# Kernel optimization log

Hardware: AMD Instinct MI355X
Metric: run time of the kernel (lower is better)

The kernel has to match this reference:

```python
import jax, jax.numpy as jnp
import numpy as np

NUM_EDGES = 2_000_000
D = 32
NODE_NUM = 100_000


def setup_inputs() -> dict:
    key = jax.random.key(0)
    k1, k2 = jax.random.split(key)
    H = jax.random.normal(k1, (NUM_EDGES, D), dtype=jnp.float32)
    X_node = jax.random.randint(k2, (NUM_EDGES,), 0, NODE_NUM, dtype=jnp.int64)
    return {"H": H, "X_node": X_node, "node_num": NODE_NUM}


def reference(H, X_node, node_num):
    # Original builds a dense one-hot mask [node_num, num_edges] and does mm(mask, H).
    # That is exactly a scatter-sum of edge features H into node buckets by X_node.
    # (Note: torch.range(0, node_num-1) == arange(node_num) for integer node_num.)
    return jax.ops.segment_sum(H, X_node, num_segments=node_num)
```

## Files before the change

### kernel.cpp

```cpp
#include <hip/hip_runtime.h>
#include <hip/hip_bf16.h>


__global__ void AggrSum_46299747451335_kernel(const float* __restrict__ H,
                                              const int* __restrict__ X_node,
                                              float* __restrict__ out,
                                              int num_edges) {
    long long t = (long long)blockIdx.x * blockDim.x + threadIdx.x;
    long long total = (long long)num_edges * 32;
    if (t >= total) return;
    int edge = (int)(t >> 5);
    int col  = (int)(t & 31);
    int node = X_node[edge];
    float v = H[t];
    unsafeAtomicAdd(&out[(long long)node * 32 + col], v);
}

extern "C" void kernel_launch(void* const* d_in, const int* in_sizes, int n_in,
                              void* d_out, int out_size, void* d_ws, size_t ws_size,
                              hipStream_t stream) {
    const float* H      = (const float*)d_in[0];
    const int*   X_node = (const int*)d_in[1];
    float*       out    = (float*)d_out;

    const int num_edges = in_sizes[0] / 32;

    hipMemsetAsync(d_out, 0, (size_t)out_size * sizeof(float), stream);

    long long total_threads = (long long)num_edges * 32;
    int block = 256;
    long long grid = (total_threads + block - 1) / block;
    AggrSum_46299747451335_kernel<<<(dim3)(unsigned)grid, block, 0, stream>>>(
        H, X_node, out, num_edges);
}
```

Before: 458.6 us.

## Bucket edges by node bin and accumulate per-bin in shared memory

Replaces the global-atomic scatter-sum with a counting-sort pipeline: histogram edges into bins of 64 nodes, scan the counts, scatter edge indices into bin order, then have one block per bin sum H rows into shared-memory accumulators and write each output once. This removes the global float atomics and the output memset. In exchange it adds four launches, needs workspace, uses global atomics on the bin cursors (which is contended), and reads H at random row addresses. It falls back to the old kernel when the workspace or the size limits are not met.

```diff
diff --git a/kernel.cpp b/kernel.cpp
--- a/kernel.cpp
+++ b/kernel.cpp
@@ -1,6 +1,90 @@
 #include <hip/hip_runtime.h>
-#include <hip/hip_bf16.h>
 
+
+#define NPB   64
+#define SHIFT 6
+#define MAXBINS 2048
+
+__global__ void hist_kernel(const int* __restrict__ X, int E,
+                            int* __restrict__ counts, int nbins) {
+    extern __shared__ int h[];
+    for (int i = threadIdx.x; i < nbins; i += blockDim.x) h[i] = 0;
+    __syncthreads();
+    int stride = gridDim.x * blockDim.x;
+    for (long long i = (long long)blockIdx.x * blockDim.x + threadIdx.x; i < E;
+         i += stride)
+        atomicAdd(&h[X[i] >> SHIFT], 1);
+    __syncthreads();
+    for (int i = threadIdx.x; i < nbins; i += blockDim.x) {
+        int c = h[i];
+        if (c) atomicAdd(&counts[i], c);
+    }
+}
+
+__global__ void scan_kernel(const int* __restrict__ counts,
+                            int* __restrict__ start,
+                            int* __restrict__ cursor, int nbins) {
+    __shared__ int s[1024];
+    int tid = threadIdx.x;
+    int i0 = 2 * tid, i1 = 2 * tid + 1;
+    int c0 = (i0 < nbins) ? counts[i0] : 0;
+    int c1 = (i1 < nbins) ? counts[i1] : 0;
+    int pair = c0 + c1;
+    s[tid] = pair;
+    __syncthreads();
+    for (int off = 1; off < 1024; off <<= 1) {
+        int add = (tid >= off) ? s[tid - off] : 0;
+        __syncthreads();
+        s[tid] += add;
+        __syncthreads();
+    }
+    int excl = s[tid] - pair;
+    if (i0 < nbins) { start[i0] = excl;      cursor[i0] = excl;      }
+    if (i1 < nbins) { start[i1] = excl + c0; cursor[i1] = excl + c0; }
+}
+
+__global__ void scatter_kernel(const int* __restrict__ X, int E,
+                               int* __restrict__ cursor,
+                               unsigned* __restrict__ sorted) {
+    long long i = (long long)blockIdx.x * blockDim.x + threadIdx.x;
+    if (i >= E) return;
+    int node = X[(int)i];
+    int bin  = node >> SHIFT;
+    int pos  = atomicAdd(&cursor[bin], 1);
+    sorted[pos] = (unsigned)i | ((unsigned)(node & (NPB - 1)) << 24);
+}
+
+__global__ __launch_bounds__(256) void gather_kernel(
+        const float* __restrict__ H,
+        const unsigned* __restrict__ sorted,
+        const int* __restrict__ start,
+        float* __restrict__ out,
+        int E, int nbins, int nnodes) {
+    __shared__ float acc[NPB * 32];
+    int bin = blockIdx.x;
+    int s   = start[bin];
+    int end = (bin + 1 < nbins) ? start[bin + 1] : E;
+
+    for (int i = threadIdx.x; i < NPB * 32; i += 256) acc[i] = 0.0f;
+    __syncthreads();
+
+    int col  = threadIdx.x & 31;
+    int slot = threadIdx.x >> 5;
+    for (int i = s + slot; i < end; i += 8) {
+        unsigned p = sorted[i];
+        int edge  = (int)(p & 0xFFFFFFu);
+        int local = (int)(p >> 24);
+        float v = H[(long long)edge * 32 + col];
+        unsafeAtomicAdd(&acc[local * 32 + col], v);
+    }
+    __syncthreads();
+
+    int node_base = bin << SHIFT;
+    for (int i = threadIdx.x; i < NPB * 32; i += 256) {
+        int node = node_base + (i >> 5);
+        if (node < nnodes) out[(long long)node * 32 + (i & 31)] = acc[i];
+    }
+}
 
 __global__ void AggrSum_46299747451335_kernel(const float* __restrict__ H,
                                               const int* __restrict__ X_node,
@@ -24,12 +108,37 @@
     float*       out    = (float*)d_out;
 
     const int num_edges = in_sizes[0] / 32;
+    const int num_nodes = out_size / 32;
+    const int nbins     = (num_nodes + NPB - 1) >> SHIFT;
 
-    hipMemsetAsync(d_out, 0, (size_t)out_size * sizeof(float), stream);
+    size_t need = (size_t)3 * MAXBINS * sizeof(int)
+                + (size_t)num_edges * sizeof(unsigned);
 
-    long long total_threads = (long long)num_edges * 32;
-    int block = 256;
-    long long grid = (total_threads + block - 1) / block;
-    AggrSum_46299747451335_kernel<<<(dim3)(unsigned)grid, block, 0, stream>>>(
-        H, X_node, out, num_edges);
+    if (nbins <= MAXBINS && num_edges < (1 << 24) && ws_size >= need) {
+        char* ws = (char*)d_ws;
+        int*      counts = (int*)(ws);
+        int*      start  = (int*)(ws + (size_t)MAXBINS * sizeof(int));
+        int*      cursor = (int*)(ws + (size_t)2 * MAXBINS * sizeof(int));
+        unsigned* sorted = (unsigned*)(ws + (size_t)3 * MAXBINS * sizeof(int));
+
+        hipMemsetAsync(counts, 0, (size_t)nbins * sizeof(int), stream);
+
+        hist_kernel<<<256, 256, nbins * sizeof(int), stream>>>(
+            X_node, num_edges, counts, nbins);
+
+        scan_kernel<<<1, 1024, 0, stream>>>(counts, start, cursor, nbins);
+
+        int sgrid = (num_edges + 255) / 256;
+        scatter_kernel<<<sgrid, 256, 0, stream>>>(X_node, num_edges, cursor, sorted);
+
+        gather_kernel<<<nbins, 256, 0, stream>>>(
+            H, sorted, start, out, num_edges, nbins, num_nodes);
+    } else {
+        hipMemsetAsync(d_out, 0, (size_t)out_size * sizeof(float), stream);
+        long long total_threads = (long long)num_edges * 32;
+        int block = 256;
+        long long grid = (total_threads + block - 1) / block;
+        AggrSum_46299747451335_kernel<<<(dim3)(unsigned)grid, block, 0, stream>>>(
+            H, X_node, out, num_edges);
+    }
 }
```

Result: slower. 977.2 us (+113.1%).

## Replace global atomic scatter with binned counting sort and LDS gather-accumulate

Applied to the files above, without the earlier changes.

Edges are bucketed by node block (64 nodes per bin) through a histogram, a two-level scan and a scatter into a sorted index array. Each gather block then accumulates its bin's edges into shared memory and writes the output once, so the global float atomics and the output memset go away. The cost is several extra launches, workspace use, and random row gathers from H during the gather. If the workspace is too small or the sizes exceed the bounds, it falls back to the old atomic kernel.

```diff
diff --git a/kernel.cpp b/kernel.cpp
--- a/kernel.cpp
+++ b/kernel.cpp
@@ -1,6 +1,130 @@
 #include <hip/hip_runtime.h>
-#include <hip/hip_bf16.h>
 
+
+#define NPB     64
+#define SHIFT   6
+#define MAXBINS 2048
+#define NB      256
+
+__global__ __launch_bounds__(1024) void hist_kernel(
+        const int* __restrict__ X, int E, int chunk,
+        int* __restrict__ hist, int nbins) {
+    __shared__ int h[MAXBINS];
+    int blk = blockIdx.x;
+    for (int b = threadIdx.x; b < nbins; b += 1024) h[b] = 0;
+    __syncthreads();
+    int beg = blk * chunk;
+    int end = min(beg + chunk, E);
+    for (int i = beg + threadIdx.x; i < end; i += 1024)
+        atomicAdd(&h[X[i] >> SHIFT], 1);
+    __syncthreads();
+    for (int b = threadIdx.x; b < nbins; b += 1024)
+        hist[b * NB + blk] = h[b];
+}
+
+__global__ __launch_bounds__(256) void scanA_kernel(
+        int* __restrict__ hist, int* __restrict__ binTotal) {
+    __shared__ int s[NB];
+    int b = blockIdx.x, tid = threadIdx.x;
+    int v = hist[b * NB + tid];
+    s[tid] = v;
+    __syncthreads();
+    for (int off = 1; off < NB; off <<= 1) {
+        int add = (tid >= off) ? s[tid - off] : 0;
+        __syncthreads();
+        s[tid] += add;
+        __syncthreads();
+    }
+    hist[b * NB + tid] = s[tid] - v;
+    if (tid == NB - 1) binTotal[b] = s[NB - 1];
+}
+
+__global__ __launch_bounds__(1024) void scanB_kernel(
+        const int* __restrict__ binTotal, int* __restrict__ binStart,
+        int nbins) {
+    __shared__ int s[1024];
+    int tid = threadIdx.x;
+    int i0 = 2 * tid, i1 = 2 * tid + 1;
+    int c0 = (i0 < nbins) ? binTotal[i0] : 0;
+    int c1 = (i1 < nbins) ? binTotal[i1] : 0;
+    int pair = c0 + c1;
+    s[tid] = pair;
+    __syncthreads();
+    for (int off = 1; off < 1024; off <<= 1) {
+        int add = (tid >= off) ? s[tid - off] : 0;
+        __syncthreads();
+        s[tid] += add;
+        __syncthreads();
+    }
+    int excl = s[tid] - pair;
+    if (i0 < nbins) binStart[i0] = excl;
+    if (i1 < nbins) binStart[i1] = excl + c0;
+    if (tid == 1023) binStart[nbins] = s[1023];
+}
+
+__global__ __launch_bounds__(1024) void scatter_kernel(
+        const int* __restrict__ X, int E, int chunk,
+        const int* __restrict__ hist, const int* __restrict__ binStart,
+        unsigned* __restrict__ sorted, int nbins) {
+    __shared__ int cur[MAXBINS];
+    int blk = blockIdx.x;
+    for (int b = threadIdx.x; b < nbins; b += 1024)
+        cur[b] = binStart[b] + hist[b * NB + blk];
+    __syncthreads();
+    int beg = blk * chunk;
+    int end = min(beg + chunk, E);
+    for (int i = beg + threadIdx.x; i < end; i += 1024) {
+        int node = X[i];
+        int b = node >> SHIFT;
+        int pos = atomicAdd(&cur[b], 1);
+        sorted[pos] = (unsigned)i | ((unsigned)(node & (NPB - 1)) << 24);
+    }
+}
+
+__global__ __launch_bounds__(256) void gather_kernel(
+        const float* __restrict__ H,
+        const unsigned* __restrict__ sorted,
+        const int* __restrict__ binStart,
+        float* __restrict__ out,
+        int nbins, int nnodes) {
+    __shared__ float acc[NPB * 32];
+    int bin = blockIdx.x;
+    int s   = binStart[bin];
+    int end = binStart[bin + 1];
+
+    for (int i = threadIdx.x; i < NPB * 32; i += 256) acc[i] = 0.0f;
+    __syncthreads();
+
+    int col = threadIdx.x & 31;
+    int grp = threadIdx.x >> 5;
+    int i = s + grp;
+    for (; i + 24 < end; i += 32) {
+        unsigned p0 = sorted[i];
+        unsigned p1 = sorted[i + 8];
+        unsigned p2 = sorted[i + 16];
+        unsigned p3 = sorted[i + 24];
+        float v0 = H[(long long)(p0 & 0xFFFFFFu) * 32 + col];
+        float v1 = H[(long long)(p1 & 0xFFFFFFu) * 32 + col];
+        float v2 = H[(long long)(p2 & 0xFFFFFFu) * 32 + col];
+        float v3 = H[(long long)(p3 & 0xFFFFFFu) * 32 + col];
+        unsafeAtomicAdd(&acc[(p0 >> 24) * 32 + col], v0);
+        unsafeAtomicAdd(&acc[(p1 >> 24) * 32 + col], v1);
+        unsafeAtomicAdd(&acc[(p2 >> 24) * 32 + col], v2);
+        unsafeAtomicAdd(&acc[(p3 >> 24) * 32 + col], v3);
+    }
+    for (; i < end; i += 8) {
+        unsigned p = sorted[i];
+        float v = H[(long long)(p & 0xFFFFFFu) * 32 + col];
+        unsafeAtomicAdd(&acc[(p >> 24) * 32 + col], v);
+    }
+    __syncthreads();
+
+    int node_base = bin << SHIFT;
+    for (int i2 = threadIdx.x; i2 < NPB * 32; i2 += 256) {
+        int node = node_base + (i2 >> 5);
+        if (node < nnodes) out[(long long)node * 32 + (i2 & 31)] = acc[i2];
+    }
+}
 
 __global__ void AggrSum_46299747451335_kernel(const float* __restrict__ H,
                                               const int* __restrict__ X_node,
@@ -24,12 +148,37 @@
     float*       out    = (float*)d_out;
 
     const int num_edges = in_sizes[0] / 32;
+    const int num_nodes = out_size / 32;
+    const int nbins     = (num_nodes + NPB - 1) >> SHIFT;
+    const int chunk     = (num_edges + NB - 1) / NB;
 
-    hipMemsetAsync(d_out, 0, (size_t)out_size * sizeof(float), stream);
+    size_t off_hist   = 0;
+    size_t off_total  = off_hist  + (size_t)MAXBINS * NB * sizeof(int);
+    size_t off_start  = off_total + (size_t)MAXBINS * sizeof(int);
+    size_t off_sorted = off_start + (size_t)(MAXBINS + 1) * sizeof(int);
+    size_t need       = off_sorted + (size_t)num_edges * sizeof(unsigned);
 
-    long long total_threads = (long long)num_edges * 32;
-    int block = 256;
-    long long grid = (total_threads + block - 1) / block;
-    AggrSum_46299747451335_kernel<<<(dim3)(unsigned)grid, block, 0, stream>>>(
-        H, X_node, out, num_edges);
+    if (nbins <= MAXBINS && num_edges < (1 << 24) && ws_size >= need) {
+        char* ws = (char*)d_ws;
+        int*      hist     = (int*)(ws + off_hist);
+        int*      binTotal = (int*)(ws + off_total);
+        int*      binStart = (int*)(ws + off_start);
+        unsigned* sorted   = (unsigned*)(ws + off_sorted);
+
+        hist_kernel<<<NB, 1024, 0, stream>>>(X_node, num_edges, chunk,
+                                             hist, nbins);
+        scanA_kernel<<<nbins, NB, 0, stream>>>(hist, binTotal);
+        scanB_kernel<<<1, 1024, 0, stream>>>(binTotal, binStart, nbins);
+        scatter_kernel<<<NB, 1024, 0, stream>>>(X_node, num_edges, chunk,
+                                                hist, binStart, sorted, nbins);
+        gather_kernel<<<nbins, 256, 0, stream>>>(H, sorted, binStart, out,
+                                                 nbins, num_nodes);
+    } else {
+        hipMemsetAsync(d_out, 0, (size_t)out_size * sizeof(float), stream);
+        long long total_threads = (long long)num_edges * 32;
+        int block = 256;
+        long long grid = (total_threads + block - 1) / block;
+        AggrSum_46299747451335_kernel<<<(dim3)(unsigned)grid, block, 0, stream>>>(
+            H, X_node, out, num_edges);
+    }
 }
```

Measured after the change: 667.2 us. 45.5% more time.
